# Kernel optimization log

Measured on AMD Instinct MI355X. Metric: run time of the kernel, lower is better.

The kernel has to match this reference:

```python
import jax, jax.numpy as jnp
import numpy as np

N_CELLS = 50000
HID = 64
DEG = 16
K_NODES = 4  # nodes per cell; cell i owns nodes [4i, 4i+4)
SP = 3


def setup_inputs() -> dict:
    key = jax.random.key(0)
    ks = jax.random.split(key, 12)
    s = 1.0 / np.sqrt(HID)
    inp = {
        'features': jax.random.normal(ks[0], (N_CELLS, HID), jnp.float32),
        'positions': jax.random.normal(ks[1], (K_NODES * N_CELLS, SP), jnp.float32),
        'neighbors': jax.random.randint(ks[2], (N_CELLS, DEG), 0, N_CELLS, jnp.int32),
        # message MLP: Linear(2H+1 -> H), SiLU, Linear(H -> H)
        'W1': jax.random.normal(ks[3], (2 * HID + 1, HID), jnp.float32) * s,
        'b1': jnp.zeros((HID,), jnp.float32),
        'W2': jax.random.normal(ks[4], (HID, HID), jnp.float32) * s,
        'b2': jnp.zeros((HID,), jnp.float32),
        # update MLP: Linear(H + H -> H), SiLU, Linear(H -> H)
        'Wu1': jax.random.normal(ks[5], (2 * HID, HID), jnp.float32) * s,
        'bu1': jnp.zeros((HID,), jnp.float32),
        'Wu2': jax.random.normal(ks[6], (HID, HID), jnp.float32) * s,
        'bu2': jnp.zeros((HID,), jnp.float32),
    }
    return inp


def reference(features, positions, neighbors, W1, b1, W2, b2, Wu1, bu1, Wu2, bu2):
    N, H = features.shape
    # centroid of each cell's owned nodes (cell i -> nodes [K*i, K*i+K))
    cent = positions.reshape(N, K_NODES, SP).mean(axis=1)          # [N, sp]
    fj = features[neighbors]                                       # [N, D, H]
    cj = cent[neighbors]                                           # [N, D, sp]
    # centroid-distance geometric invariant per (cell, neighbor) pair
    geom = jnp.linalg.norm(cent[:, None, :] - cj, axis=-1, keepdims=True)  # [N, D, 1]
    fi = jnp.broadcast_to(features[:, None, :], fj.shape)          # [N, D, H]
    x = jnp.concatenate([fi, fj, geom], axis=-1)                   # [N, D, 2H+1]
    h = jax.nn.silu(x @ W1 + b1) @ W2 + b2                         # [N, D, H]
    msg = h.mean(axis=1)                                           # mean over neighbors
    u = jnp.concatenate([features, msg], axis=-1)                  # [N, 2H]
    upd = jax.nn.silu(u @ Wu1 + bu1) @ Wu2 + bu2
    updated_features = features + upd
    return updated_features, positions
```

## Files before the change

### kernel.cpp

```cpp
#include <hip/hip_runtime.h>


#define DEG 16

typedef __attribute__((ext_vector_type(8))) short short8;
typedef __attribute__((ext_vector_type(4))) float f32x4;
typedef uint2 uint2_a __attribute__((may_alias));
typedef uint4 uint4_a __attribute__((may_alias));

union HbRd { uint4_a u; short8 s; };
union Frag { short8 s; uint4 u; };

__device__ __forceinline__ unsigned f2bf(float f) {
  unsigned u = __float_as_uint(f);
  return (u + 0x7FFFu + ((u >> 16) & 1u)) >> 16;
}
__device__ __forceinline__ float bf2f(unsigned bits16) {
  return __uint_as_float(bits16 << 16);
}
__device__ __forceinline__ float silu(float h) {
  return h / (1.f + __expf(-h));
}
__device__ __forceinline__ float silu_fast(float h) {
  return h * __builtin_amdgcn_rcpf(1.f + __expf(-h));
}

__global__ __launch_bounds__(256) void aux_kernel(
    const float* __restrict__ pos,
    const float* __restrict__ W1, const float* __restrict__ W2,
    const float* __restrict__ Wu1, const float* __restrict__ Wu2,
    float* __restrict__ outpos,
    unsigned short* __restrict__ w1pq, unsigned short* __restrict__ w2t,
    unsigned short* __restrict__ wu1t, unsigned short* __restrict__ wu2b)
{
  int t = blockIdx.x * 256 + threadIdx.x;
  if (t < 150000) {
    ((float4*)outpos)[t] = ((const float4*)pos)[t];
  } else if (t < 174576) {
    const int r = t - 150000;
    if (r < 8192) {
      const int j = r & 7, l = (r >> 3) & 15, q = (r >> 7) & 3;
      const int f = r >> 9, kk = f & 1, mt = f >> 1;
      const int k = kk * 32 + q * 8 + j;
      const int m = mt * 16 + l;
      w1pq[r] = (unsigned short)f2bf(
          (m < 64) ? W1[k * 64 + m] : W1[(k + 64) * 64 + (m - 64)]);
    } else if (r < 12288) {
      const int s = r - 8192;
      const int j = s & 7, l = (s >> 3) & 15, q = (s >> 7) & 3;
      const int f = s >> 9, kk = f & 1, mt = f >> 1;
      const int k = kk * 32 + q * 8 + j;
      w2t[s] = (unsigned short)f2bf(W2[k * 64 + mt * 16 + l]);
    } else if (r < 20480) {
      const int s = r - 12288;
      const int j = s & 7, l = (s >> 3) & 15, q = (s >> 7) & 3;
      const int f = s >> 9, kk = f & 3, mt = f >> 2;
      const int k = kk * 32 + q * 8 + j;
      wu1t[s] = (unsigned short)f2bf(Wu1[k * 64 + mt * 16 + l]);
    } else {
      const int s = r - 20480;
      const int j = s & 7, l = (s >> 3) & 15, q = (s >> 7) & 3;
      const int f = s >> 9, kk = f & 1, nt = f >> 1;
      const int k = kk * 32 + q * 8 + j;
      wu2b[s] = (unsigned short)f2bf(Wu2[k * 64 + nt * 16 + l]);
    }
  }
}

__global__ __launch_bounds__(256) void prep_pq_kernel(
    const float* __restrict__ feat, const float* __restrict__ pos,
    const unsigned short* __restrict__ w1pq,
    unsigned short* __restrict__ featb, float* __restrict__ cent4,
    unsigned short* __restrict__ Pb, unsigned char* __restrict__ Q8)
{
  const int lane = threadIdx.x & 63;
  const int wid  = threadIdx.x >> 6;
  const int quad = lane >> 4;
  const int l15  = lane & 15;

  const int tile = blockIdx.x * 4 + wid;
  const bool act = (tile < 3125);
  const int  tt  = act ? tile : 3124;
  const int  cr  = tt * 16 + l15;

  short8 xf[2];
  #pragma unroll
  for (int kk = 0; kk < 2; ++kk) {
    const float4 f0 = *(const float4*)(feat + cr * 64 + kk * 32 + quad * 8);
    const float4 f1 = *(const float4*)(feat + cr * 64 + kk * 32 + quad * 8 + 4);
    Frag v;
    v.s[0] = (short)f2bf(f0.x); v.s[1] = (short)f2bf(f0.y);
    v.s[2] = (short)f2bf(f0.z); v.s[3] = (short)f2bf(f0.w);
    v.s[4] = (short)f2bf(f1.x); v.s[5] = (short)f2bf(f1.y);
    v.s[6] = (short)f2bf(f1.z); v.s[7] = (short)f2bf(f1.w);
    xf[kk] = v.s;
    if (act) *(uint4*)(featb + cr * 64 + kk * 32 + quad * 8) = v.u;
  }

  if (act && lane < 16) {
    const float4* pp = (const float4*)(pos + 12 * cr);
    const float4 a = pp[0], b = pp[1], c = pp[2];
    float4 o;
    o.x = (a.x + a.w + b.z + c.y) * 0.25f;
    o.y = (a.y + b.x + b.w + c.z) * 0.25f;
    o.z = (a.z + b.y + c.x + c.w) * 0.25f;
    o.w = 0.f;
    ((float4*)cent4)[cr] = o;
  }

  short8 wf[8][2];
  #pragma unroll
  for (int mt = 0; mt < 8; ++mt)
    #pragma unroll
    for (int kk = 0; kk < 2; ++kk)
      wf[mt][kk] = *(const short8*)(w1pq + (((mt * 2 + kk) * 4 + quad) << 7) + l15 * 8);

  f32x4 acc[8] = {};
  #pragma unroll
  for (int kk = 0; kk < 2; ++kk)
    #pragma unroll
    for (int mt = 0; mt < 8; ++mt)
      acc[mt] = __builtin_amdgcn_mfma_f32_16x16x32_bf16(wf[mt][kk], xf[kk], acc[mt], 0, 0, 0);

  if (act) {
    #pragma unroll
    for (int mt = 0; mt < 4; ++mt) {
      uint2 pk;
      pk.x = f2bf(acc[mt][0]) | (f2bf(acc[mt][1]) << 16);
      pk.y = f2bf(acc[mt][2]) | (f2bf(acc[mt][3]) << 16);
      *(uint2*)(Pb + cr * 64 + mt * 16 + quad * 4) = pk;
    }
    #pragma unroll
    for (int mt = 4; mt < 8; ++mt) {
      int w = __builtin_amdgcn_cvt_pk_fp8_f32(acc[mt][0], acc[mt][1], 0, false);
      w = __builtin_amdgcn_cvt_pk_fp8_f32(acc[mt][2], acc[mt][3], w, true);
      *(unsigned int*)(Q8 + cr * 64 + (mt - 4) * 16 + quad * 4) = (unsigned)w;
    }
  }
}

__global__ __launch_bounds__(256) void gather_kernel(
    const unsigned short* __restrict__ Pb,
    const unsigned char* __restrict__ Q8,
    const float4* __restrict__ cent4,
    const int* __restrict__ nbr,
    const float* __restrict__ b1, const float* __restrict__ W1,
    unsigned short* __restrict__ sB)
{
  const int lane = threadIdx.x & 63;
  const int wid  = threadIdx.x >> 6;
  const int c    = blockIdx.x * 4 + wid;

  const int nj = nbr[c * DEG + (lane & 15)];

  const float4 ci = cent4[c];
  const float4 cj = cent4[nj];
  const float dx = ci.x - cj.x, dy = ci.y - cj.y, dz = ci.z - cj.z;
  const float g = sqrtf(dx * dx + dy * dy + dz * dz);

  const float pcb = bf2f(Pb[c * 64 + lane]) + b1[lane];
  const float wl  = W1[8192 + lane];

  float acc = 0.f;
  #pragma unroll
  for (int d = 0; d < DEG; ++d) {
    const int   nd = __builtin_amdgcn_readlane(nj, d);
    const float gd = __uint_as_float(
        __builtin_amdgcn_readlane((int)__float_as_uint(g), d));
    const float qv = __builtin_amdgcn_cvt_f32_fp8((int)Q8[nd * 64 + lane], 0);
    acc += silu_fast(pcb + qv + gd * wl);
  }

  sB[c * 64 + lane] = (unsigned short)f2bf(acc * 0.0625f);
}

__global__ __launch_bounds__(256) void tail_kernel(
    const unsigned short* __restrict__ featb,
    const unsigned short* __restrict__ sB,
    const float* __restrict__ feat,
    const unsigned short* __restrict__ w2t,
    const unsigned short* __restrict__ wu1t,
    const unsigned short* __restrict__ wu2b,
    const float* __restrict__ b2, const float* __restrict__ bu1,
    const float* __restrict__ bu2,
    float* __restrict__ outf)
{
  __shared__ uint4 smem[4 * 288];
  const int lane = threadIdx.x & 63;
  const int wid  = threadIdx.x >> 6;
  const int quad = lane >> 4;
  const int l15  = lane & 15;
  char* Msg = (char*)(smem + wid * 288);
  char* Hb  = Msg + 2304;

  short8 w2f[4][2];
  #pragma unroll
  for (int mt = 0; mt < 4; ++mt)
    #pragma unroll
    for (int kk = 0; kk < 2; ++kk)
      w2f[mt][kk] = *(const short8*)(w2t + (((mt * 2 + kk) * 4 + quad) << 7) + l15 * 8);
  short8 wu1f[4][4];
  #pragma unroll
  for (int mt = 0; mt < 4; ++mt)
    #pragma unroll
    for (int kk = 0; kk < 4; ++kk)
      wu1f[mt][kk] = *(const short8*)(wu1t + (((mt * 4 + kk) * 4 + quad) << 7) + l15 * 8);
  short8 wu2f[4][2];
  #pragma unroll
  for (int nt = 0; nt < 4; ++nt)
    #pragma unroll
    for (int kk = 0; kk < 2; ++kk)
      wu2f[nt][kk] = *(const short8*)(wu2b + (((nt * 2 + kk) * 4 + quad) << 7) + l15 * 8);

  f32x4 b2f[4], bu1f[4];
  #pragma unroll
  for (int mt = 0; mt < 4; ++mt) {
    b2f[mt]  = *(const f32x4*)(b2  + mt * 16 + quad * 4);
    bu1f[mt] = *(const f32x4*)(bu1 + mt * 16 + quad * 4);
  }
  float bu2v[4];
  #pragma unroll
  for (int nt = 0; nt < 4; ++nt) bu2v[nt] = bu2[nt * 16 + l15];

  const int tile = blockIdx.x * 4 + wid;
  const bool act = (tile < 3125);
  const int  tt  = act ? tile : 3124;
  const int  cr  = tt * 16 + l15;

  f32x4 accm[4] = {};
  #pragma unroll
  for (int kk = 0; kk < 2; ++kk) {
    const short8 bf = *(const short8*)(sB + cr * 64 + kk * 32 + quad * 8);
    #pragma unroll
    for (int mt = 0; mt < 4; ++mt)
      accm[mt] = __builtin_amdgcn_mfma_f32_16x16x32_bf16(w2f[mt][kk], bf, accm[mt], 0, 0, 0);
  }
  #pragma unroll
  for (int mt = 0; mt < 4; ++mt) {
    uint2 pk;
    pk.x = f2bf(accm[mt][0] + b2f[mt][0]) | (f2bf(accm[mt][1] + b2f[mt][1]) << 16);
    pk.y = f2bf(accm[mt][2] + b2f[mt][2]) | (f2bf(accm[mt][3] + b2f[mt][3]) << 16);
    *(uint2_a*)(Msg + l15 * 144 + mt * 32 + quad * 8) = pk;
  }
  __threadfence_block();

  f32x4 accu[4] = {};
  #pragma unroll
  for (int kk = 0; kk < 4; ++kk) {
    short8 bf;
    if (kk < 2) {
      bf = *(const short8*)(featb + cr * 64 + kk * 32 + quad * 8);
    } else {
      HbRd t; t.u = *(const uint4_a*)(Msg + l15 * 144 + (kk - 2) * 64 + quad * 16);
      bf = t.s;
    }
    #pragma unroll
    for (int mt = 0; mt < 4; ++mt)
      accu[mt] = __builtin_amdgcn_mfma_f32_16x16x32_bf16(wu1f[mt][kk], bf, accu[mt], 0, 0, 0);
  }
  #pragma unroll
  for (int mt = 0; mt < 4; ++mt) {
    float sv[4];
    #pragma unroll
    for (int rg = 0; rg < 4; ++rg)
      sv[rg] = silu(accu[mt][rg] + bu1f[mt][rg]);
    uint2 pk;
    pk.x = f2bf(sv[0]) | (f2bf(sv[1]) << 16);
    pk.y = f2bf(sv[2]) | (f2bf(sv[3]) << 16);
    *(uint2_a*)(Hb + l15 * 144 + mt * 32 + quad * 8) = pk;
  }
  __threadfence_block();

  f32x4 acc2[4] = {};
  #pragma unroll
  for (int kk = 0; kk < 2; ++kk) {
    HbRd t; t.u = *(const uint4_a*)(Hb + l15 * 144 + kk * 64 + quad * 16);
    const short8 af = t.s;
    #pragma unroll
    for (int nt = 0; nt < 4; ++nt)
      acc2[nt] = __builtin_amdgcn_mfma_f32_16x16x32_bf16(af, wu2f[nt][kk], acc2[nt], 0, 0, 0);
  }
  if (act) {
    #pragma unroll
    for (int nt = 0; nt < 4; ++nt)
      #pragma unroll
      for (int rg = 0; rg < 4; ++rg) {
        const int row = tt * 16 + quad * 4 + rg;
        const int col = nt * 16 + l15;
        outf[row * 64 + col] = feat[row * 64 + col] + acc2[nt][rg] + bu2v[nt];
      }
  }
}

extern "C" void kernel_launch(void* const* d_in, const int* in_sizes, int n_in,
                              void* d_out, int out_size, void* d_ws, size_t ws_size,
                              hipStream_t stream)
{
  const float* feat = (const float*)d_in[0];
  const float* pos  = (const float*)d_in[1];
  const int*   nbr  = (const int*)d_in[2];
  const float* W1   = (const float*)d_in[3];
  const float* b1   = (const float*)d_in[4];
  const float* W2   = (const float*)d_in[5];
  const float* b2   = (const float*)d_in[6];
  const float* Wu1  = (const float*)d_in[7];
  const float* bu1  = (const float*)d_in[8];
  const float* Wu2  = (const float*)d_in[9];
  const float* bu2  = (const float*)d_in[10];
  float* out = (float*)d_out;

  unsigned short* featb = (unsigned short*)d_ws;
  unsigned short* Pb    = (unsigned short*)((char*)d_ws + 6400000);
  unsigned char*  Q8    = (unsigned char*)((char*)d_ws + 12800000);
  unsigned short* sB    = (unsigned short*)((char*)d_ws + 19200000);
  float*          cent4 = (float*)((char*)d_ws + 25600000);
  unsigned short* w1pq  = (unsigned short*)((char*)d_ws + 26400000);
  unsigned short* w2t   = (unsigned short*)((char*)d_ws + 26416384);
  unsigned short* wu1t  = (unsigned short*)((char*)d_ws + 26424576);
  unsigned short* wu2b  = (unsigned short*)((char*)d_ws + 26440960);

  aux_kernel<<<682, 256, 0, stream>>>(pos, W1, W2, Wu1, Wu2, out + 3200000,
                                      w1pq, w2t, wu1t, wu2b);
  prep_pq_kernel<<<782, 256, 0, stream>>>(feat, pos, w1pq, featb, cent4,
                                          Pb, Q8);
  gather_kernel<<<12500, 256, 0, stream>>>(Pb, Q8, (const float4*)cent4, nbr,
                                           b1, W1, sB);
  tail_kernel<<<782, 256, 0, stream>>>(featb, sB, feat, w2t, wu1t, wu2b,
                                       b2, bu1, bu2, out);
}
```

Measured before the change: 132.4 us.

## Precompute centroid distances in prep kernel, move centroid calc to aux kernel

Centroid computation moves into the aux kernel. The prep kernel gains extra blocks that compute the per-pair centroid distances into a geomF buffer. The gather kernel then reads precomputed distances instead of doing a random cent4 gather and sqrt per neighbor. This takes the random centroid gather off the gather kernel's critical path and runs it alongside the MFMA prep work. In exchange it writes and reads an extra 3.2MB buffer.

```diff
diff --git a/kernel.cpp b/kernel.cpp
--- a/kernel.cpp
+++ b/kernel.cpp
@@ -29,7 +29,7 @@
     const float* __restrict__ pos,
     const float* __restrict__ W1, const float* __restrict__ W2,
     const float* __restrict__ Wu1, const float* __restrict__ Wu2,
-    float* __restrict__ outpos,
+    float* __restrict__ outpos, float* __restrict__ cent4,
     unsigned short* __restrict__ w1pq, unsigned short* __restrict__ w2t,
     unsigned short* __restrict__ wu1t, unsigned short* __restrict__ wu2b)
 {
@@ -64,21 +64,48 @@
       const int k = kk * 32 + q * 8 + j;
       wu2b[s] = (unsigned short)f2bf(Wu2[k * 64 + nt * 16 + l]);
     }
-  }
-}
-
-__global__ __launch_bounds__(256) void prep_pq_kernel(
-    const float* __restrict__ feat, const float* __restrict__ pos,
+  } else if (t < 224576) {
+    const int i = t - 174576;
+    const float4* pp = (const float4*)(pos + 12 * i);
+    const float4 a = pp[0], b = pp[1], c = pp[2];
+    float4 o;
+    o.x = (a.x + a.w + b.z + c.y) * 0.25f;
+    o.y = (a.y + b.x + b.w + c.z) * 0.25f;
+    o.z = (a.z + b.y + c.x + c.w) * 0.25f;
+    o.w = 0.f;
+    ((float4*)cent4)[i] = o;
+  }
+}
+
+__global__ __launch_bounds__(256) void prep_geom_kernel(
+    const float* __restrict__ feat,
     const unsigned short* __restrict__ w1pq,
-    unsigned short* __restrict__ featb, float* __restrict__ cent4,
-    unsigned short* __restrict__ Pb, unsigned char* __restrict__ Q8)
-{
+    const float4* __restrict__ cent4,
+    const int* __restrict__ nbr,
+    unsigned short* __restrict__ featb,
+    unsigned short* __restrict__ Pb, unsigned char* __restrict__ Q8,
+    float* __restrict__ geomF)
+{
+  const int b    = blockIdx.x;
   const int lane = threadIdx.x & 63;
   const int wid  = threadIdx.x >> 6;
+
+  if (b >= 782) {
+    const int gb  = b - 782;
+    const int sub = lane >> 4;
+    const int d   = lane & 15;
+    const int c   = gb * 16 + wid * 4 + sub;
+    const int nj  = nbr[c * DEG + d];
+    const float4 ci = cent4[c];
+    const float4 cj = cent4[nj];
+    const float dx = ci.x - cj.x, dy = ci.y - cj.y, dz = ci.z - cj.z;
+    geomF[c * DEG + d] = sqrtf(dx * dx + dy * dy + dz * dz);
+    return;
+  }
+
   const int quad = lane >> 4;
   const int l15  = lane & 15;
-
-  const int tile = blockIdx.x * 4 + wid;
+  const int tile = b * 4 + wid;
   const bool act = (tile < 3125);
   const int  tt  = act ? tile : 3124;
   const int  cr  = tt * 16 + l15;
@@ -97,17 +124,6 @@
     if (act) *(uint4*)(featb + cr * 64 + kk * 32 + quad * 8) = v.u;
   }
 
-  if (act && lane < 16) {
-    const float4* pp = (const float4*)(pos + 12 * cr);
-    const float4 a = pp[0], b = pp[1], c = pp[2];
-    float4 o;
-    o.x = (a.x + a.w + b.z + c.y) * 0.25f;
-    o.y = (a.y + b.x + b.w + c.z) * 0.25f;
-    o.z = (a.z + b.y + c.x + c.w) * 0.25f;
-    o.w = 0.f;
-    ((float4*)cent4)[cr] = o;
-  }
-
   short8 wf[8][2];
   #pragma unroll
   for (int mt = 0; mt < 8; ++mt)
@@ -142,7 +158,7 @@
 __global__ __launch_bounds__(256) void gather_kernel(
     const unsigned short* __restrict__ Pb,
     const unsigned char* __restrict__ Q8,
-    const float4* __restrict__ cent4,
+    const float* __restrict__ geomF,
     const int* __restrict__ nbr,
     const float* __restrict__ b1, const float* __restrict__ W1,
     unsigned short* __restrict__ sB)
@@ -151,12 +167,8 @@
   const int wid  = threadIdx.x >> 6;
   const int c    = blockIdx.x * 4 + wid;
 
-  const int nj = nbr[c * DEG + (lane & 15)];
-
-  const float4 ci = cent4[c];
-  const float4 cj = cent4[nj];
-  const float dx = ci.x - cj.x, dy = ci.y - cj.y, dz = ci.z - cj.z;
-  const float g = sqrtf(dx * dx + dy * dy + dz * dz);
+  const int   nj = nbr[c * DEG + (lane & 15)];
+  const float gv = geomF[c * DEG + (lane & 15)];
 
   const float pcb = bf2f(Pb[c * 64 + lane]) + b1[lane];
   const float wl  = W1[8192 + lane];
@@ -166,7 +178,7 @@
   for (int d = 0; d < DEG; ++d) {
     const int   nd = __builtin_amdgcn_readlane(nj, d);
     const float gd = __uint_as_float(
-        __builtin_amdgcn_readlane((int)__float_as_uint(g), d));
+        __builtin_amdgcn_readlane((int)__float_as_uint(gv), d));
     const float qv = __builtin_amdgcn_cvt_f32_fp8((int)Q8[nd * 64 + lane], 0);
     acc += silu_fast(pcb + qv + gd * wl);
   }
@@ -312,6 +324,7 @@
   unsigned short* featb = (unsigned short*)d_ws;
   unsigned short* Pb    = (unsigned short*)((char*)d_ws + 6400000);
   unsigned char*  Q8    = (unsigned char*)((char*)d_ws + 12800000);
+  float*          geomF = (float*)((char*)d_ws + 16000000);
   unsigned short* sB    = (unsigned short*)((char*)d_ws + 19200000);
   float*          cent4 = (float*)((char*)d_ws + 25600000);
   unsigned short* w1pq  = (unsigned short*)((char*)d_ws + 26400000);
@@ -319,12 +332,11 @@
   unsigned short* wu1t  = (unsigned short*)((char*)d_ws + 26424576);
   unsigned short* wu2b  = (unsigned short*)((char*)d_ws + 26440960);
 
-  aux_kernel<<<682, 256, 0, stream>>>(pos, W1, W2, Wu1, Wu2, out + 3200000,
-                                      w1pq, w2t, wu1t, wu2b);
-  prep_pq_kernel<<<782, 256, 0, stream>>>(feat, pos, w1pq, featb, cent4,
-                                          Pb, Q8);
-  gather_kernel<<<12500, 256, 0, stream>>>(Pb, Q8, (const float4*)cent4, nbr,
-                                           b1, W1, sB);
+  aux_kernel<<<878, 256, 0, stream>>>(pos, W1, W2, Wu1, Wu2, out + 3200000,
+                                      cent4, w1pq, w2t, wu1t, wu2b);
+  prep_geom_kernel<<<3907, 256, 0, stream>>>(feat, w1pq, (const float4*)cent4,
+                                             nbr, featb, Pb, Q8, geomF);
+  gather_kernel<<<12500, 256, 0, stream>>>(Pb, Q8, geomF, nbr, b1, W1, sB);
   tail_kernel<<<782, 256, 0, stream>>>(featb, sB, feat, w2t, wu1t, wu2b,
                                        b2, bu1, bu2, out);
 }
```

Result: no change. 132.4 us (-0.0%).
